# Optimization experiments

Hardware: AMD Instinct MI355X
Metric: run time of the kernel (lower is better)

## Reference

```python
import jax, jax.numpy as jnp
import numpy as np

EPS = 1e-12


def setup_inputs() -> dict:
    key = jax.random.key(0)
    k1, k2, k3, k4 = jax.random.split(key, 4)
    B, S, IN_DIM, OUT_DIM = 8, 4096, 1024, 256
    return {
        "psi_re": jax.random.normal(k1, (B, S, IN_DIM), dtype=jnp.float32),
        "psi_im": jax.random.normal(k2, (B, S, IN_DIM), dtype=jnp.float32),
        "basis_re": jax.random.normal(k3, (OUT_DIM, IN_DIM), dtype=jnp.float32) * 0.02,
        "basis_im": jax.random.normal(k4, (OUT_DIM, IN_DIM), dtype=jnp.float32) * 0.02,
    }


def reference(psi_re, psi_im, basis_re, basis_im):
    # Assemble complex64 state and measurement basis
    psi = jax.lax.complex(psi_re, psi_im)            # (B, S, in_dim) complex64
    basis = jax.lax.complex(basis_re, basis_im)      # (out_dim, in_dim) complex64

    # inner = psi @ basis^H : amplitudes <phi_m | psi>
    inner = jnp.einsum("bsi,mi->bsm", psi, jnp.conj(basis))  # (B, S, out_dim)

    # Born-rule normalize: P(m) = |inner|^2 / sum_m |inner|^2
    p = jnp.real(inner) ** 2 + jnp.imag(inner) ** 2          # |z|^2, real fp32
    probs = p / (jnp.sum(p, axis=-1, keepdims=True) + EPS)   # (B, S, out_dim)

    # collapsed = sum_m P(m) * |phi_m>  ==  probs @ basis
    collapsed = jnp.einsum("bsm,mi->bsi", probs.astype(jnp.complex64), basis)

    # Renormalize to unit quantum state: psi / ||psi||_2
    norm = jnp.sqrt(jnp.sum(jnp.real(collapsed) ** 2 + jnp.imag(collapsed) ** 2,
                            axis=-1, keepdims=True))
    collapsed = collapsed / (norm + EPS).astype(jnp.complex64)
    return collapsed, probs
```

## Files before the change

kernel.cpp:

```cpp
#include <hip/hip_runtime.h>
#include <math.h>

#define IN_DIM 1024
#define M_DIM  256
#define R_TOT  32768
#define TM     32
#define EPS    1e-12f
#define BSTRIDE 144
#define PROW   1040


typedef __attribute__((ext_vector_type(8))) short s16x8;
typedef __attribute__((ext_vector_type(4))) float f32x4;

union FragU { int i[4]; int4 i4; s16x8 v; };

#define MFMA16 __builtin_amdgcn_mfma_f32_16x16x32_bf16

__device__ __forceinline__ int cvt_pk_bf16(float lo, float hi) {
    int r;
    asm("v_cvt_pk_bf16_f32 %0, %1, %2" : "=v"(r) : "v"(lo), "v"(hi));
    return r;
}
__device__ __forceinline__ unsigned short rtn_bf16(float x) {
    unsigned u = __float_as_uint(x);
    return (unsigned short)((u + 0x7FFFu + ((u >> 16) & 1u)) >> 16);
}

__global__ __launch_bounds__(256, 3) void povm_kernel(
    const float* __restrict__ psi_re, const float* __restrict__ psi_im,
    const float* __restrict__ basis_re, const float* __restrict__ basis_im,
    float* __restrict__ out,
    long long off_im,
    long long off_probs,
    long long cap)
{
    __shared__ __align__(16) char sMem[M_DIM * BSTRIDE];
    __shared__ float sRS[4][TM];
    __shared__ float sScale[TM];

    const int tid  = threadIdx.x;
    const int lane = tid & 63;
    const int w    = tid >> 6;
    const int g    = lane >> 4;
    const int h16  = lane & 15;
    const int row0 = blockIdx.x * TM;
    const int mw   = w * 64;

    const int sq  = tid & 3;
    const int smb = tid >> 2;

    f32x4 accRe[2][4], accIm[2][4];
    #pragma unroll
    for (int rt = 0; rt < 2; ++rt)
        #pragma unroll
        for (int ct = 0; ct < 4; ++ct) {
            accRe[rt][ct] = (f32x4){0.f, 0.f, 0.f, 0.f};
            accIm[rt][ct] = (f32x4){0.f, 0.f, 0.f, 0.f};
        }

    for (int ks = 0; ks < 64; ++ks) {
        const int ib = ks * 16;

        float4 ar[2], ai[2];
        #pragma unroll
        for (int rt = 0; rt < 2; ++rt) {
            const size_t off = (size_t)(row0 + rt * 16 + h16) * IN_DIM + ib + g * 4;
            ar[rt] = *(const float4*)(psi_re + off);
            ai[rt] = *(const float4*)(psi_im + off);
        }

        #pragma unroll
        for (int it = 0; it < 4; ++it) {
            const int m = it * 64 + smb;
            const size_t boff = (size_t)m * IN_DIM + ib + sq * 4;
            const float4 br = *(const float4*)(basis_re + boff);
            const float4 bi = *(const float4*)(basis_im + boff);
            FragU hf, lf;
            #pragma unroll
            for (int d = 0; d < 4; ++d) {
                const float re = (&br.x)[d], im = (&bi.x)[d];
                const unsigned ur = __float_as_uint(re), ui = __float_as_uint(im);
                hf.i[d] = (int)((ur >> 16) | (ui & 0xFFFF0000u));
                const float lr = re - __uint_as_float(ur & 0xFFFF0000u);
                const float li = im - __uint_as_float(ui & 0xFFFF0000u);
                lf.i[d] = (int)((__float_as_uint(lr) >> 16) |
                                (__float_as_uint(li) & 0xFFFF0000u));
            }
            char* rowp = sMem + m * BSTRIDE;
            *(int4*)(rowp + 16 * sq)      = hf.i4;
            *(int4*)(rowp + 64 + 16 * sq) = lf.i4;
        }
        __syncthreads();

        s16x8 a1h[2], a1l[2], a2h[2], a2l[2];
        #pragma unroll
        for (int rt = 0; rt < 2; ++rt) {
            FragU fh, fl, gh, gl;
            #pragma unroll
            for (int d = 0; d < 4; ++d) {
                const float re = (&ar[rt].x)[d], im = (&ai[rt].x)[d];
                const unsigned ur = __float_as_uint(re), ui = __float_as_uint(im);
                fh.i[d] = (int)((ur >> 16) | (ui & 0xFFFF0000u));
                const float lr = re - __uint_as_float(ur & 0xFFFF0000u);
                const float li = im - __uint_as_float(ui & 0xFFFF0000u);
                fl.i[d] = (int)((__float_as_uint(lr) >> 16) |
                                (__float_as_uint(li) & 0xFFFF0000u));
                const unsigned x = (unsigned)fh.i[d];
                gh.i[d] = (int)(((x >> 16) | (x << 16)) ^ 0x80000000u);
                const unsigned y = (unsigned)fl.i[d];
                gl.i[d] = (int)(((y >> 16) | (y << 16)) ^ 0x80000000u);
            }
            a1h[rt] = fh.v; a1l[rt] = fl.v;
            a2h[rt] = gh.v; a2l[rt] = gl.v;
        }

        #pragma unroll
        for (int ct = 0; ct < 4; ++ct) {
            const char* rowp = sMem + (mw + ct * 16 + h16) * BSTRIDE;
            const s16x8 bh = *(const s16x8*)(rowp + 16 * g);
            const s16x8 bl = *(const s16x8*)(rowp + 64 + 16 * g);
            #pragma unroll
            for (int rt = 0; rt < 2; ++rt) {
                accRe[rt][ct] = MFMA16(a1h[rt], bh, accRe[rt][ct], 0, 0, 0);
                accRe[rt][ct] = MFMA16(a1h[rt], bl, accRe[rt][ct], 0, 0, 0);
                accRe[rt][ct] = MFMA16(a1l[rt], bh, accRe[rt][ct], 0, 0, 0);
                accIm[rt][ct] = MFMA16(a2h[rt], bh, accIm[rt][ct], 0, 0, 0);
                accIm[rt][ct] = MFMA16(a2h[rt], bl, accIm[rt][ct], 0, 0, 0);
                accIm[rt][ct] = MFMA16(a2l[rt], bh, accIm[rt][ct], 0, 0, 0);
            }
        }
        __syncthreads();
    }

    float rs[2][4];
    #pragma unroll
    for (int rt = 0; rt < 2; ++rt)
        #pragma unroll
        for (int q = 0; q < 4; ++q) rs[rt][q] = 0.f;
    #pragma unroll
    for (int rt = 0; rt < 2; ++rt)
        #pragma unroll
        for (int ct = 0; ct < 4; ++ct)
            #pragma unroll
            for (int q = 0; q < 4; ++q) {
                const float p = accRe[rt][ct][q] * accRe[rt][ct][q] +
                                accIm[rt][ct][q] * accIm[rt][ct][q];
                accRe[rt][ct][q] = p;
                rs[rt][q] += p;
            }
    #pragma unroll
    for (int off = 1; off < 16; off <<= 1) {
        #pragma unroll
        for (int rt = 0; rt < 2; ++rt)
            #pragma unroll
            for (int q = 0; q < 4; ++q)
                rs[rt][q] += __shfl_xor(rs[rt][q], off, 64);
    }
    if (h16 == 0) {
        #pragma unroll
        for (int rt = 0; rt < 2; ++rt)
            #pragma unroll
            for (int q = 0; q < 4; ++q)
                sRS[w][rt * 16 + g * 4 + q] = rs[rt][q];
    }
    __syncthreads();
    float inv[2][4];
    #pragma unroll
    for (int rt = 0; rt < 2; ++rt)
        #pragma unroll
        for (int q = 0; q < 4; ++q) {
            const int R = rt * 16 + g * 4 + q;
            inv[rt][q] = 1.f / (sRS[0][R] + sRS[1][R] + sRS[2][R] + sRS[3][R] + EPS);
        }
    #pragma unroll
    for (int rt = 0; rt < 2; ++rt)
        #pragma unroll
        for (int ct = 0; ct < 4; ++ct)
            #pragma unroll
            for (int q = 0; q < 4; ++q) {
                const float p = accRe[rt][ct][q] * inv[rt][q];
                const int R  = rt * 16 + g * 4 + q;
                const int Mc = mw + ct * 16 + h16;
                const unsigned short ph = rtn_bf16(p);
                const float phf = __uint_as_float((unsigned)ph << 16);
                const unsigned short pl = rtn_bf16(p - phf);
                *(unsigned short*)(sMem + R * PROW + 2 * Mc)       = ph;
                *(unsigned short*)(sMem + R * PROW + 512 + 2 * Mc) = pl;
                const long long po = off_probs + (long long)(row0 + R) * M_DIM + Mc;
                if (po < cap) out[po] = p;
            }
    __syncthreads();

    {
        const int wi0 = w * 256;
        float nsqp[2][4];
        #pragma unroll
        for (int rt = 0; rt < 2; ++rt)
            #pragma unroll
            for (int q = 0; q < 4; ++q) nsqp[rt][q] = 0.f;

        for (int ibk = 0; ibk < 4; ++ibk) {
            const int ibase = wi0 + ibk * 64;
            f32x4 cRe[2][4], cIm[2][4];
            #pragma unroll
            for (int rt = 0; rt < 2; ++rt)
                #pragma unroll
                for (int nt = 0; nt < 4; ++nt) {
                    cRe[rt][nt] = (f32x4){0.f, 0.f, 0.f, 0.f};
                    cIm[rt][nt] = (f32x4){0.f, 0.f, 0.f, 0.f};
                }
            for (int ks = 0; ks < 8; ++ks) {
                s16x8 ah[2], al[2];
                #pragma unroll
                for (int rt = 0; rt < 2; ++rt) {
                    const char* rp = sMem + (rt * 16 + h16) * PROW + ks * 64 + 16 * g;
                    ah[rt] = *(const s16x8*)(rp);
                    al[rt] = *(const s16x8*)(rp + 512);
                }
                const int mrow = ks * 32 + 8 * g;
                #pragma unroll
                for (int nt = 0; nt < 4; ++nt) {
                    const int col = ibase + nt * 16 + h16;
                    const float* pr = basis_re + (size_t)mrow * IN_DIM + col;
                    const float* pi = basis_im + (size_t)mrow * IN_DIM + col;
                    FragU bR, bI;
                    #pragma unroll
                    for (int d = 0; d < 4; ++d) {
                        bR.i[d] = cvt_pk_bf16(pr[(size_t)(2 * d) * IN_DIM],
                                              pr[(size_t)(2 * d + 1) * IN_DIM]);
                        bI.i[d] = cvt_pk_bf16(pi[(size_t)(2 * d) * IN_DIM],
                                              pi[(size_t)(2 * d + 1) * IN_DIM]);
                    }
                    #pragma unroll
                    for (int rt = 0; rt < 2; ++rt) {
                        cRe[rt][nt] = MFMA16(ah[rt], bR.v, cRe[rt][nt], 0, 0, 0);
                        cRe[rt][nt] = MFMA16(al[rt], bR.v, cRe[rt][nt], 0, 0, 0);
                        cIm[rt][nt] = MFMA16(ah[rt], bI.v, cIm[rt][nt], 0, 0, 0);
                        cIm[rt][nt] = MFMA16(al[rt], bI.v, cIm[rt][nt], 0, 0, 0);
                    }
                }
            }
            #pragma unroll
            for (int rt = 0; rt < 2; ++rt)
                #pragma unroll
                for (int nt = 0; nt < 4; ++nt) {
                    const int col = ibase + nt * 16 + h16;
                    #pragma unroll
                    for (int q = 0; q < 4; ++q) {
                        const float vr = cRe[rt][nt][q], vi = cIm[rt][nt][q];
                        nsqp[rt][q] += vr * vr + vi * vi;
                        const int row = rt * 16 + 4 * g + q;
                        const long long o = (long long)(row0 + row) * IN_DIM + col;
                        if (o < off_im) out[o] = vr;
                        const long long oi = off_im + o;
                        if (oi < off_probs) out[oi] = vi;
                    }
                }
        }
        #pragma unroll
        for (int off = 1; off < 16; off <<= 1) {
            #pragma unroll
            for (int rt = 0; rt < 2; ++rt)
                #pragma unroll
                for (int q = 0; q < 4; ++q)
                    nsqp[rt][q] += __shfl_xor(nsqp[rt][q], off, 64);
        }
        if (h16 == 0) {
            #pragma unroll
            for (int rt = 0; rt < 2; ++rt)
                #pragma unroll
                for (int q = 0; q < 4; ++q)
                    sRS[w][rt * 16 + 4 * g + q] = nsqp[rt][q];
        }
        __syncthreads();
        if (tid < TM)
            sScale[tid] = 1.f / (sqrtf(sRS[0][tid] + sRS[1][tid] +
                                       sRS[2][tid] + sRS[3][tid]) + EPS);
        __syncthreads();
    }

    {
        const int tr = tid >> 5;
        const int tm = tid & 31;
        for (int ic = 0; ic < 4; ++ic) {
            const int i0 = ic * 256 + 8 * tm;
            #pragma unroll
            for (int a = 0; a < 4; ++a) {
                const int row = 4 * tr + a;
                const float s = sScale[row];
                const long long o = (long long)(row0 + row) * IN_DIM + i0;
                if (o + 8 <= off_im) {
                    #pragma unroll
                    for (int q = 0; q < 2; ++q) {
                        float4 v = *(float4*)(out + o + 4 * q);
                        v.x *= s; v.y *= s; v.z *= s; v.w *= s;
                        *(float4*)(out + o + 4 * q) = v;
                    }
                }
                const long long oi = off_im + o;
                if (oi + 8 <= off_probs) {
                    #pragma unroll
                    for (int q = 0; q < 2; ++q) {
                        float4 vw = *(float4*)(out + oi + 4 * q);
                        vw.x *= s; vw.y *= s; vw.z *= s; vw.w *= s;
                        *(float4*)(out + oi + 4 * q) = vw;
                    }
                }
            }
        }
    }
}

extern "C" void kernel_launch(void* const* d_in, const int* in_sizes, int n_in,
                              void* d_out, int out_size, void* d_ws, size_t ws_size,
                              hipStream_t stream)
{
    const float* psi_re   = (const float*)d_in[0];
    const float* psi_im   = (const float*)d_in[1];
    const float* basis_re = (const float*)d_in[2];
    const float* basis_im = (const float*)d_in[3];

    const long long RIN = (long long)R_TOT * IN_DIM;
    const long long RM  = (long long)R_TOT * M_DIM;
    const long long cap = (long long)out_size;

    long long off_im, off_probs;
    if (cap == 2 * RIN + RM) {
        off_im = RIN; off_probs = 2 * RIN;
    } else if (cap == RIN + RM) {
        off_im = RIN; off_probs = RIN;
    } else {
        long long plane = (cap - RM) / 2;
        if (plane < 0) plane = 0;
        off_im = plane; off_probs = 2 * plane;
    }

    povm_kernel<<<R_TOT / TM, 256, 0, stream>>>(psi_re, psi_im, basis_re, basis_im,
                                                (float*)d_out, off_im, off_probs, cap);
}
```

Before: 972.0 us.

## Prefetch next k-slice into registers and use hardware bf16 conversion for splits

Adds software prefetching so that the psi and basis global loads for the next k-step are issued before the current step's conversion and MFMA work, which hides global memory latency. The bf16 hi/lo split now uses v_cvt_pk_bf16_f32 (round-to-nearest) in place of manual truncation masks, and the first __syncthreads moves after the A-fragment conversion. This increases register pressure from the double-buffered float4 registers and slightly changes the rounding of the split.

```diff
diff --git a/kernel.cpp b/kernel.cpp
--- a/kernel.cpp
+++ b/kernel.cpp
@@ -59,39 +59,56 @@
             accIm[rt][ct] = (f32x4){0.f, 0.f, 0.f, 0.f};
         }
 
+    float4 car[2], cai[2], cbr[4], cbi[4];
+    {
+        #pragma unroll
+        for (int rt = 0; rt < 2; ++rt) {
+            const size_t off = (size_t)(row0 + rt * 16 + h16) * IN_DIM + g * 4;
+            car[rt] = *(const float4*)(psi_re + off);
+            cai[rt] = *(const float4*)(psi_im + off);
+        }
+        #pragma unroll
+        for (int it = 0; it < 4; ++it) {
+            const size_t boff = (size_t)(it * 64 + smb) * IN_DIM + sq * 4;
+            cbr[it] = *(const float4*)(basis_re + boff);
+            cbi[it] = *(const float4*)(basis_im + boff);
+        }
+    }
+
     for (int ks = 0; ks < 64; ++ks) {
-        const int ib = ks * 16;
-
-        float4 ar[2], ai[2];
-        #pragma unroll
-        for (int rt = 0; rt < 2; ++rt) {
-            const size_t off = (size_t)(row0 + rt * 16 + h16) * IN_DIM + ib + g * 4;
-            ar[rt] = *(const float4*)(psi_re + off);
-            ai[rt] = *(const float4*)(psi_im + off);
+        float4 nar[2], nai[2], nbr[4], nbi[4];
+        if (ks < 63) {
+            const int ibn = (ks + 1) * 16;
+            #pragma unroll
+            for (int rt = 0; rt < 2; ++rt) {
+                const size_t off = (size_t)(row0 + rt * 16 + h16) * IN_DIM + ibn + g * 4;
+                nar[rt] = *(const float4*)(psi_re + off);
+                nai[rt] = *(const float4*)(psi_im + off);
+            }
+            #pragma unroll
+            for (int it = 0; it < 4; ++it) {
+                const size_t boff = (size_t)(it * 64 + smb) * IN_DIM + ibn + sq * 4;
+                nbr[it] = *(const float4*)(basis_re + boff);
+                nbi[it] = *(const float4*)(basis_im + boff);
+            }
         }
 
         #pragma unroll
         for (int it = 0; it < 4; ++it) {
-            const int m = it * 64 + smb;
-            const size_t boff = (size_t)m * IN_DIM + ib + sq * 4;
-            const float4 br = *(const float4*)(basis_re + boff);
-            const float4 bi = *(const float4*)(basis_im + boff);
             FragU hf, lf;
             #pragma unroll
             for (int d = 0; d < 4; ++d) {
-                const float re = (&br.x)[d], im = (&bi.x)[d];
-                const unsigned ur = __float_as_uint(re), ui = __float_as_uint(im);
-                hf.i[d] = (int)((ur >> 16) | (ui & 0xFFFF0000u));
-                const float lr = re - __uint_as_float(ur & 0xFFFF0000u);
-                const float li = im - __uint_as_float(ui & 0xFFFF0000u);
-                lf.i[d] = (int)((__float_as_uint(lr) >> 16) |
-                                (__float_as_uint(li) & 0xFFFF0000u));
-            }
-            char* rowp = sMem + m * BSTRIDE;
+                const float re = (&cbr[it].x)[d], im = (&cbi[it].x)[d];
+                const int wh = cvt_pk_bf16(re, im);
+                const float reh = __uint_as_float(((unsigned)wh) << 16);
+                const float imh = __uint_as_float(((unsigned)wh) & 0xFFFF0000u);
+                hf.i[d] = wh;
+                lf.i[d] = cvt_pk_bf16(re - reh, im - imh);
+            }
+            char* rowp = sMem + (it * 64 + smb) * BSTRIDE;
             *(int4*)(rowp + 16 * sq)      = hf.i4;
             *(int4*)(rowp + 64 + 16 * sq) = lf.i4;
         }
-        __syncthreads();
 
         s16x8 a1h[2], a1l[2], a2h[2], a2l[2];
         #pragma unroll
@@ -99,21 +116,21 @@
             FragU fh, fl, gh, gl;
             #pragma unroll
             for (int d = 0; d < 4; ++d) {
-                const float re = (&ar[rt].x)[d], im = (&ai[rt].x)[d];
-                const unsigned ur = __float_as_uint(re), ui = __float_as_uint(im);
-                fh.i[d] = (int)((ur >> 16) | (ui & 0xFFFF0000u));
-                const float lr = re - __uint_as_float(ur & 0xFFFF0000u);
-                const float li = im - __uint_as_float(ui & 0xFFFF0000u);
-                fl.i[d] = (int)((__float_as_uint(lr) >> 16) |
-                                (__float_as_uint(li) & 0xFFFF0000u));
-                const unsigned x = (unsigned)fh.i[d];
+                const float re = (&car[rt].x)[d], im = (&cai[rt].x)[d];
+                const int wh = cvt_pk_bf16(re, im);
+                const float reh = __uint_as_float(((unsigned)wh) << 16);
+                const float imh = __uint_as_float(((unsigned)wh) & 0xFFFF0000u);
+                const int wl = cvt_pk_bf16(re - reh, im - imh);
+                fh.i[d] = wh; fl.i[d] = wl;
+                const unsigned x = (unsigned)wh;
                 gh.i[d] = (int)(((x >> 16) | (x << 16)) ^ 0x80000000u);
-                const unsigned y = (unsigned)fl.i[d];
+                const unsigned y = (unsigned)wl;
                 gl.i[d] = (int)(((y >> 16) | (y << 16)) ^ 0x80000000u);
             }
             a1h[rt] = fh.v; a1l[rt] = fl.v;
             a2h[rt] = gh.v; a2l[rt] = gl.v;
         }
+        __syncthreads();
 
         #pragma unroll
         for (int ct = 0; ct < 4; ++ct) {
@@ -131,6 +148,13 @@
             }
         }
         __syncthreads();
+
+        if (ks < 63) {
+            #pragma unroll
+            for (int rt = 0; rt < 2; ++rt) { car[rt] = nar[rt]; cai[rt] = nai[rt]; }
+            #pragma unroll
+            for (int it = 0; it < 4; ++it) { cbr[it] = nbr[it]; cbi[it] = nbi[it]; }
+        }
     }
 
     float rs[2][4];
```

Result: slower. 1.084 ms (+11.5%).
